# Kernel tuning notes

Hardware: AMD Instinct MI355X
Metric: run time of the kernel (lower is better)

The kernel has to match this reference:

```python
import jax, jax.numpy as jnp
import numpy as np

N, E, F_IN, HID, H, EDIM, G = 50000, 800000, 64, 32, 4, 4, 1024
NEG = 0.2  # LeakyReLU slope (GATv2Conv default)


def _glorot(key, shape):
    s = jnp.sqrt(6.0 / (shape[0] + shape[-1]))
    return jax.random.uniform(key, shape, minval=-s, maxval=s, dtype=jnp.float32)


def setup_inputs() -> dict:
    key = jax.random.key(0)
    ks = jax.random.split(key, 20)
    d = {}
    d["x"] = jax.random.normal(ks[0], (N, F_IN), dtype=jnp.float32)
    d["edge_index"] = jax.random.randint(ks[1], (2, E), 0, N)
    d["edge_attr"] = jax.random.normal(ks[2], (E, EDIM), dtype=jnp.float32)
    d["batch"] = jnp.sort(jax.random.randint(ks[3], (N,), 0, G))
    dims = [F_IN, HID * H, HID * H]
    i = 4
    for l, din in enumerate(dims, 1):
        d[f"Wl{l}"] = _glorot(ks[i], (din, H * HID)); i += 1
        d[f"bl{l}"] = jnp.zeros((H * HID,), jnp.float32)
        d[f"Wr{l}"] = _glorot(ks[i], (din, H * HID)); i += 1
        d[f"br{l}"] = jnp.zeros((H * HID,), jnp.float32)
        d[f"We{l}"] = _glorot(ks[i], (EDIM, H * HID)); i += 1
        d[f"att{l}"] = _glorot(ks[i], (H, HID)); i += 1
        d[f"bias{l}"] = jnp.zeros((H * HID,), jnp.float32)
    d["Wlin"] = _glorot(ks[i], (H * HID, 1)); i += 1
    d["blin"] = jnp.zeros((1,), jnp.float32)
    return d


def _add_self_loops(edge_index, edge_attr):
    # PyG add_self_loops with fill_value='mean': self-loop edge feature is the
    # mean of incoming-edge features (zeros for isolated targets).
    src0, dst0 = edge_index[0], edge_index[1]
    cnt = jax.ops.segment_sum(jnp.ones((src0.shape[0],), jnp.float32), dst0, num_segments=N)
    loop_attr = jax.ops.segment_sum(edge_attr, dst0, num_segments=N) / jnp.maximum(cnt, 1.0)[:, None]
    ar = jnp.arange(N)
    src = jnp.concatenate([src0, ar])
    dst = jnp.concatenate([dst0, ar])
    ea = jnp.concatenate([edge_attr, loop_attr], axis=0)
    return src, dst, ea


def _gatv2_conv(x, src, dst, ea, Wl, bl, Wr, br, We, att, bias):
    n = x.shape[0]
    xl = (x @ Wl + bl).reshape(n, H, HID)   # source transform (message values)
    xr = (x @ Wr + br).reshape(n, H, HID)   # target transform
    e = jax.nn.leaky_relu(xl[src] + xr[dst] + (ea @ We).reshape(-1, H, HID), NEG)  # [Etot,H,C]
    logit = jnp.einsum('ehc,hc->eh', e, att)
    # segment softmax over destination node (every node has a self-loop)
    m = jax.ops.segment_max(logit, dst, num_segments=n)
    p = jnp.exp(logit - m[dst])
    s = jax.ops.segment_sum(p, dst, num_segments=n)
    alpha = p / (s[dst] + 1e-16)
    out = jax.ops.segment_sum(alpha[:, :, None] * xl[src], dst, num_segments=n)
    return out.reshape(n, H * HID) + bias


def reference(x, edge_index, edge_attr, batch,
              Wl1, bl1, Wr1, br1, We1, att1, bias1,
              Wl2, bl2, Wr2, br2, We2, att2, bias2,
              Wl3, bl3, Wr3, br3, We3, att3, bias3,
              Wlin, blin):
    src, dst, ea = _add_self_loops(edge_index, edge_attr)
    h = jax.nn.relu(_gatv2_conv(x, src, dst, ea, Wl1, bl1, Wr1, br1, We1, att1, bias1))
    h = jax.nn.relu(_gatv2_conv(h, src, dst, ea, Wl2, bl2, Wr2, br2, We2, att2, bias2))
    h = _gatv2_conv(h, src, dst, ea, Wl3, bl3, Wr3, br3, We3, att3, bias3)
    # global mean pool over graphs
    cnt = jax.ops.segment_sum(jnp.ones((N,), jnp.float32), batch, num_segments=G)
    pooled = jax.ops.segment_sum(h, batch, num_segments=G) / jnp.maximum(cnt, 1.0)[:, None]
    # dropout p=0.35 is identity in eval mode
    return pooled @ Wlin + blin
```

## Files before the change

### kernel.cpp

```cpp
#include <hip/hip_runtime.h>
#include <math.h>

#define NN 50000
#define EE 800000
#define FIN 64
#define GG 1024
#define ETOT (EE + NN)
#define PSLOT 16

typedef float v2f __attribute__((ext_vector_type(2)));

__global__ __launch_bounds__(256) void k_init(int* __restrict__ deg, int* __restrict__ fillpos,
    float* __restrict__ psum, int* __restrict__ pcnt) {
  int i = blockIdx.x * 256 + threadIdx.x;
  if (i < NN) { deg[i] = 0; fillpos[i] = 0; }
  if (i < GG * PSLOT) { psum[i] = 0.f; pcnt[i] = 0; }
}

__global__ __launch_bounds__(256) void k_deg(const int* __restrict__ dst, int* __restrict__ deg,
    const int* __restrict__ batch, int* __restrict__ pcnt) {
  int e = blockIdx.x * 256 + threadIdx.x;
  if (e < NN) atomicAdd(&pcnt[(batch[e] << 4) | (e & (PSLOT - 1))], 1);
  if (e >= EE) return;
  atomicAdd(&deg[dst[e]], 1);
}

__global__ __launch_bounds__(256) void k_scan1(const int* __restrict__ deg, int* __restrict__ part) {
  __shared__ int s[256];
  int i = blockIdx.x * 256 + threadIdx.x;
  s[threadIdx.x] = (i < NN) ? deg[i] + 1 : 0;
  __syncthreads();
  for (int st = 128; st > 0; st >>= 1) {
    if (threadIdx.x < st) s[threadIdx.x] += s[threadIdx.x + st];
    __syncthreads();
  }
  if (threadIdx.x == 0) part[blockIdx.x] = s[0];
}

__global__ __launch_bounds__(256) void k_scan2(int* __restrict__ part, int nb, int* __restrict__ offsets) {
  __shared__ int s[256];
  int t = threadIdx.x;
  s[t] = (t < nb) ? part[t] : 0;
  __syncthreads();
  for (int st = 1; st < 256; st <<= 1) {
    int a = (t >= st) ? s[t - st] : 0;
    __syncthreads();
    s[t] += a;
    __syncthreads();
  }
  if (t < nb) part[t] = t ? s[t - 1] : 0;
  if (t == 0) offsets[NN] = ETOT;
}

__global__ __launch_bounds__(256) void k_scan3(const int* __restrict__ deg,
    const int* __restrict__ part, int* __restrict__ offsets) {
  __shared__ int s[256];
  int t = threadIdx.x;
  int i = blockIdx.x * 256 + t;
  int v = (i < NN) ? deg[i] + 1 : 0;
  s[t] = v;
  __syncthreads();
  for (int st = 1; st < 256; st <<= 1) {
    int a = (t >= st) ? s[t - st] : 0;
    __syncthreads();
    s[t] += a;
    __syncthreads();
  }
  if (i < NN) offsets[i] = part[blockIdx.x] + s[t] - v;
}

__global__ __launch_bounds__(256) void k_fill(const int* __restrict__ src,
    const int* __restrict__ dst, const int* __restrict__ offsets,
    const int* __restrict__ deg, int* __restrict__ fillpos,
    int2* __restrict__ pr, float4* __restrict__ csr_ea,
    const float* __restrict__ edge_attr) {
  int i = blockIdx.x * 256 + threadIdx.x;
  if (i < EE) {
    int d = dst[i];
    int p = offsets[d] + atomicAdd(&fillpos[d], 1);
    pr[p] = make_int2(i, src[i]);
    csr_ea[p] = *(const float4*)(edge_attr + (size_t)i * 4);
  } else if (i < EE + NN) {
    int n = i - EE;
    int p = offsets[n] + deg[n];
    pr[p] = make_int2(EE + n, n);
  }
}

__global__ __launch_bounds__(256) void k_selfattr(const int* __restrict__ offsets,
    float4* __restrict__ csr_ea) {
  int wave = threadIdx.x >> 6, lane = threadIdx.x & 63;
  int n = blockIdx.x * 4 + wave;
  if (n >= NN) return;
  int lo = offsets[n], d = offsets[n + 1] - lo - 1;
  float4 s = make_float4(0.f, 0.f, 0.f, 0.f);
  for (int i = lane; i < d; i += 64) {
    float4 v = csr_ea[lo + i];
    s.x += v.x; s.y += v.y; s.z += v.z; s.w += v.w;
  }
  #pragma unroll
  for (int off = 1; off < 64; off <<= 1) {
    s.x += __shfl_xor(s.x, off);
    s.y += __shfl_xor(s.y, off);
    s.z += __shfl_xor(s.z, off);
    s.w += __shfl_xor(s.w, off);
  }
  if (lane == 0) {
    float inv = 1.f / fmaxf((float)d, 1.f);
    csr_ea[lo + d] = make_float4(s.x * inv, s.y * inv, s.z * inv, s.w * inv);
  }
}

__global__ __launch_bounds__(256) void k_gemm(const float* __restrict__ X, int K,
    const float* __restrict__ Wl, const float* __restrict__ bl,
    const float* __restrict__ Wr, const float* __restrict__ br,
    float* __restrict__ xl, float* __restrict__ xr) {
  __shared__ float xsT[128][36];
  int row0 = blockIdx.x * 32;
  int nf4 = 32 * K / 4;
  for (int q = threadIdx.x; q < nf4; q += 256) {
    int r = (q * 4) / K, k0 = (q * 4) % K;
    float4 v = make_float4(0.f, 0.f, 0.f, 0.f);
    int gr = row0 + r;
    if (gr < NN) v = *(const float4*)(X + (size_t)gr * K + k0);
    xsT[k0 + 0][r] = v.x;
    xsT[k0 + 1][r] = v.y;
    xsT[k0 + 2][r] = v.z;
    xsT[k0 + 3][r] = v.w;
  }
  __syncthreads();
  int lane = threadIdx.x & 63, wv = threadIdx.x >> 6;
  int c0 = lane * 4, r0 = wv * 8;
  const float* wbase = (c0 < 128) ? (Wl + c0) : (Wr + c0 - 128);
  v2f acc2[4][4];
  #pragma unroll
  for (int rp = 0; rp < 4; rp++) {
    #pragma unroll
    for (int c = 0; c < 4; c++) acc2[rp][c] = (v2f){0.f, 0.f};
  }
  #pragma unroll 4
  for (int k = 0; k < K; k++) {
    float4 w4 = *(const float4*)(wbase + (size_t)k * 128);
    float4 xa = *(const float4*)&xsT[k][r0];
    float4 xb = *(const float4*)&xsT[k][r0 + 4];
    v2f xp[4] = {{xa.x, xa.y}, {xa.z, xa.w}, {xb.x, xb.y}, {xb.z, xb.w}};
    #pragma unroll
    for (int rp = 0; rp < 4; rp++) {
      acc2[rp][0] += xp[rp] * w4.x;
      acc2[rp][1] += xp[rp] * w4.y;
      acc2[rp][2] += xp[rp] * w4.z;
      acc2[rp][3] += xp[rp] * w4.w;
    }
  }
  float4 b4 = (c0 < 128) ? *(const float4*)(bl + c0) : *(const float4*)(br + c0 - 128);
  float* obase = (c0 < 128) ? (xl + c0) : (xr + c0 - 128);
  #pragma unroll
  for (int rp = 0; rp < 4; rp++) {
    #pragma unroll
    for (int h = 0; h < 2; h++) {
      int gr = row0 + r0 + rp * 2 + h;
      if (gr < NN) {
        float4 o;
        o.x = (h ? acc2[rp][0].y : acc2[rp][0].x) + b4.x;
        o.y = (h ? acc2[rp][1].y : acc2[rp][1].x) + b4.y;
        o.z = (h ? acc2[rp][2].y : acc2[rp][2].x) + b4.z;
        o.w = (h ? acc2[rp][3].y : acc2[rp][3].x) + b4.w;
        *(float4*)(obase + (size_t)gr * 128) = o;
      }
    }
  }
}

__global__ __launch_bounds__(64) void k_attn(
    const float* __restrict__ xl, const float* __restrict__ xr,
    const int* __restrict__ offsets, const int2* __restrict__ pr,
    const float4* __restrict__ csr_ea,
    const float* __restrict__ We, const float* __restrict__ att,
    const float* __restrict__ bias, float* __restrict__ hout, int relu_flag,
    const float* __restrict__ Wlin, const int* __restrict__ batch,
    float* __restrict__ psum) {
  int lane = threadIdx.x & 63;
  int t = blockIdx.x;
  if (t >= NN) return;
  int sub = lane >> 4;
  int cl = lane & 15;
  int ch0 = cl * 8;

  v2f xr2[4], we2[4][4], at2[4];
  {
    float4 a = *(const float4*)(xr + (size_t)t * 128 + ch0);
    float4 b = *(const float4*)(xr + (size_t)t * 128 + ch0 + 4);
    xr2[0] = (v2f){a.x, a.y}; xr2[1] = (v2f){a.z, a.w};
    xr2[2] = (v2f){b.x, b.y}; xr2[3] = (v2f){b.z, b.w};
  }
  #pragma unroll
  for (int k = 0; k < 4; k++) {
    float4 a = *(const float4*)(We + k * 128 + ch0);
    float4 b = *(const float4*)(We + k * 128 + ch0 + 4);
    we2[k][0] = (v2f){a.x, a.y}; we2[k][1] = (v2f){a.z, a.w};
    we2[k][2] = (v2f){b.x, b.y}; we2[k][3] = (v2f){b.z, b.w};
  }
  {
    float4 a = *(const float4*)(att + ch0);
    float4 b = *(const float4*)(att + ch0 + 4);
    at2[0] = (v2f){a.x, a.y}; at2[1] = (v2f){a.z, a.w};
    at2[2] = (v2f){b.x, b.y}; at2[3] = (v2f){b.z, b.w};
  }

  float den = 0.f;
  v2f acc2[4];
  #pragma unroll
  for (int j = 0; j < 4; j++) acc2[j] = (v2f){0.f, 0.f};

  int lo = offsets[t], hi = offsets[t + 1];
  int p = lo + sub;
  int s0 = 0;
  float4 ea0 = make_float4(0.f, 0.f, 0.f, 0.f);
  if (p < hi) { int2 q = pr[p]; s0 = q.y; ea0 = csr_ea[p]; }

  #pragma unroll 1
  for (; p < hi; p += 4) {
    const float* xlb = xl + (size_t)s0 * 128 + ch0;
    float4 xa = *(const float4*)(xlb);
    float4 xb = *(const float4*)(xlb + 4);
    int pn = p + 4;
    int s1 = 0;
    float4 ea1 = make_float4(0.f, 0.f, 0.f, 0.f);
    if (pn < hi) { int2 q = pr[pn]; s1 = q.y; ea1 = csr_ea[pn]; }

    v2f xls2[4] = {{xa.x, xa.y}, {xa.z, xa.w}, {xb.x, xb.y}, {xb.z, xb.w}};
    v2f d2 = (v2f){0.f, 0.f};
    #pragma unroll
    for (int j = 0; j < 4; j++) {
      v2f e2 = xls2[j] + xr2[j];
      e2 += we2[0][j] * ea0.x;
      e2 += we2[1][j] * ea0.y;
      e2 += we2[2][j] * ea0.z;
      e2 += we2[3][j] * ea0.w;
      v2f mx = {fmaxf(e2.x, 0.f), fmaxf(e2.y, 0.f)};
      e2 = e2 * 0.2f + mx * 0.8f;
      d2 += e2 * at2[j];
    }
    float part = d2.x + d2.y;
    part += __shfl_xor(part, 1);
    part += __shfl_xor(part, 2);
    float pe = __expf(part);
    den += pe;
    #pragma unroll
    for (int j = 0; j < 4; j++) acc2[j] += xls2[j] * pe;
    s0 = s1; ea0 = ea1;
  }

  #pragma unroll
  for (int off = 16; off <= 32; off <<= 1) {
    den += __shfl_xor(den, off);
    #pragma unroll
    for (int j = 0; j < 4; j++) {
      v2f o;
      o.x = __shfl_xor(acc2[j].x, off);
      o.y = __shfl_xor(acc2[j].y, off);
      acc2[j] += o;
    }
  }

  if (sub == 0) {
    float inv = 1.f / (den + 1e-16f);
    v2f bs2[4];
    {
      float4 c = *(const float4*)(bias + ch0);
      float4 d = *(const float4*)(bias + ch0 + 4);
      bs2[0] = (v2f){c.x, c.y}; bs2[1] = (v2f){c.z, c.w};
      bs2[2] = (v2f){d.x, d.y}; bs2[3] = (v2f){d.z, d.w};
    }
    v2f o2[4];
    #pragma unroll
    for (int j = 0; j < 4; j++) {
      o2[j] = acc2[j] * inv + bs2[j];
      if (relu_flag) {
        o2[j].x = fmaxf(o2[j].x, 0.f);
        o2[j].y = fmaxf(o2[j].y, 0.f);
      }
    }
    if (psum == nullptr) {
      float* ob = hout + (size_t)t * 128 + ch0;
      *(float4*)(ob) = make_float4(o2[0].x, o2[0].y, o2[1].x, o2[1].y);
      *(float4*)(ob + 4) = make_float4(o2[2].x, o2[2].y, o2[3].x, o2[3].y);
    } else {
      float4 wa = *(const float4*)(Wlin + ch0);
      float4 wb = *(const float4*)(Wlin + ch0 + 4);
      v2f wl2[4] = {{wa.x, wa.y}, {wa.z, wa.w}, {wb.x, wb.y}, {wb.z, wb.w}};
      v2f pd = o2[0] * wl2[0];
      pd += o2[1] * wl2[1];
      pd += o2[2] * wl2[2];
      pd += o2[3] * wl2[3];
      float pv = pd.x + pd.y;
      pv += __shfl_xor(pv, 1);
      pv += __shfl_xor(pv, 2);
      pv += __shfl_xor(pv, 4);
      pv += __shfl_xor(pv, 8);
      if (cl == 0) atomicAdd(&psum[(batch[t] << 4) | (t & (PSLOT - 1))], pv);
    }
  }
}

__global__ __launch_bounds__(256) void k_fin(const float* __restrict__ psum,
    const int* __restrict__ pcnt, const float* __restrict__ blin, float* __restrict__ out) {
  int g = blockIdx.x * 256 + threadIdx.x;
  if (g >= GG) return;
  float s = 0.f;
  int c = 0;
  #pragma unroll
  for (int k = 0; k < PSLOT; k++) {
    s += psum[(g << 4) | k];
    c += pcnt[(g << 4) | k];
  }
  out[g] = s / fmaxf((float)c, 1.f) + blin[0];
}

extern "C" void kernel_launch(void* const* d_in, const int* in_sizes, int n_in,
                              void* d_out, int out_size, void* d_ws, size_t ws_size,
                              hipStream_t stream) {
  const float* x = (const float*)d_in[0];
  const int* ei = (const int*)d_in[1];
  const float* edge_attr = (const float*)d_in[2];
  const int* batch = (const int*)d_in[3];
  const float *Wl[3], *bl[3], *Wr[3], *br[3], *We[3], *att[3], *bias[3];
  for (int l = 0; l < 3; l++) {
    int b = 4 + l * 7;
    Wl[l] = (const float*)d_in[b + 0];
    bl[l] = (const float*)d_in[b + 1];
    Wr[l] = (const float*)d_in[b + 2];
    br[l] = (const float*)d_in[b + 3];
    We[l] = (const float*)d_in[b + 4];
    att[l] = (const float*)d_in[b + 5];
    bias[l] = (const float*)d_in[b + 6];
  }
  const float* Wlin = (const float*)d_in[25];
  const float* blin = (const float*)d_in[26];
  float* out = (float*)d_out;

  const int* src = ei;
  const int* dst = ei + EE;

  char* p = (char*)d_ws;
  size_t used = 0;
  auto carve = [&](size_t bytes) -> void* {
    void* r = p + used;
    used += (bytes + 255) & ~(size_t)255;
    return r;
  };
  int* deg = (int*)carve(NN * sizeof(int));
  int* fillpos = (int*)carve(NN * sizeof(int));
  int* offsets = (int*)carve((NN + 1) * sizeof(int));
  int* part = (int*)carve(256 * sizeof(int));
  int2* pr = (int2*)carve((size_t)ETOT * sizeof(int2));
  float4* csr_ea = (float4*)carve((size_t)ETOT * sizeof(float4));
  float* xl = (float*)carve((size_t)NN * 128 * sizeof(float));
  float* xr = (float*)carve((size_t)NN * 128 * sizeof(float));
  float* hbuf = (float*)carve((size_t)NN * 128 * sizeof(float));
  float* psum = (float*)carve(GG * PSLOT * sizeof(float));
  int* pcnt = (int*)carve(GG * PSLOT * sizeof(int));
  if (used > ws_size) return;

  const int NB = (NN + 255) / 256;

  k_init<<<NB, 256, 0, stream>>>(deg, fillpos, psum, pcnt);
  k_deg<<<(EE + 255) / 256, 256, 0, stream>>>(dst, deg, batch, pcnt);
  k_scan1<<<NB, 256, 0, stream>>>(deg, part);
  k_scan2<<<1, 256, 0, stream>>>(part, NB, offsets);
  k_scan3<<<NB, 256, 0, stream>>>(deg, part, offsets);
  k_fill<<<(EE + NN + 255) / 256, 256, 0, stream>>>(src, dst, offsets, deg, fillpos, pr, csr_ea, edge_attr);

  const int GEMM_NB = (NN + 31) / 32;
  const int NODE_NB = (NN + 3) / 4;

  k_selfattr<<<NODE_NB, 256, 0, stream>>>(offsets, csr_ea);

  k_gemm<<<GEMM_NB, 256, 0, stream>>>(x, FIN, Wl[0], bl[0], Wr[0], br[0], xl, xr);
  k_attn<<<NN, 64, 0, stream>>>(xl, xr, offsets, pr, csr_ea, We[0], att[0], bias[0], hbuf, 1,
                                nullptr, nullptr, nullptr);
  k_gemm<<<GEMM_NB, 256, 0, stream>>>(hbuf, 128, Wl[1], bl[1], Wr[1], br[1], xl, xr);
  k_attn<<<NN, 64, 0, stream>>>(xl, xr, offsets, pr, csr_ea, We[1], att[1], bias[1], hbuf, 1,
                                nullptr, nullptr, nullptr);
  k_gemm<<<GEMM_NB, 256, 0, stream>>>(hbuf, 128, Wl[2], bl[2], Wr[2], br[2], xl, xr);
  k_attn<<<NN, 64, 0, stream>>>(xl, xr, offsets, pr, csr_ea, We[2], att[2], bias[2], nullptr, 0,
                                Wlin, batch, psum);

  k_fin<<<(GG + 255) / 256, 256, 0, stream>>>(psum, pcnt, blin, out);
}
```

Baseline: 453.4 us.

## Fuse self-loop mean attributes into attention and drop CSR edge_attr copy

Removes self-loop entries from the CSR and the permuted edge_attr buffer; the attention kernel gathers edge_attr by original edge id, accumulates the mean incoming attribute, and computes the self-loop contribution at the end. This eliminates the k_selfattr pass and the edge_attr scatter in k_fill. Index prefetching is deepened by one iteration to hide the extra indirection. The trade-off is random 16-byte gathers of edge_attr in each of three layers instead of contiguous reads.

```diff
diff --git a/kernel.cpp b/kernel.cpp
--- a/kernel.cpp
+++ b/kernel.cpp
@@ -5,7 +5,6 @@
 #define EE 800000
 #define FIN 64
 #define GG 1024
-#define ETOT (EE + NN)
 #define PSLOT 16
 
 typedef float v2f __attribute__((ext_vector_type(2)));
@@ -28,7 +27,7 @@
 __global__ __launch_bounds__(256) void k_scan1(const int* __restrict__ deg, int* __restrict__ part) {
   __shared__ int s[256];
   int i = blockIdx.x * 256 + threadIdx.x;
-  s[threadIdx.x] = (i < NN) ? deg[i] + 1 : 0;
+  s[threadIdx.x] = (i < NN) ? deg[i] : 0;
   __syncthreads();
   for (int st = 128; st > 0; st >>= 1) {
     if (threadIdx.x < st) s[threadIdx.x] += s[threadIdx.x + st];
@@ -49,7 +48,7 @@
     __syncthreads();
   }
   if (t < nb) part[t] = t ? s[t - 1] : 0;
-  if (t == 0) offsets[NN] = ETOT;
+  if (t == 0) offsets[NN] = EE;
 }
 
 __global__ __launch_bounds__(256) void k_scan3(const int* __restrict__ deg,
@@ -57,7 +56,7 @@
   __shared__ int s[256];
   int t = threadIdx.x;
   int i = blockIdx.x * 256 + t;
-  int v = (i < NN) ? deg[i] + 1 : 0;
+  int v = (i < NN) ? deg[i] : 0;
   s[t] = v;
   __syncthreads();
   for (int st = 1; st < 256; st <<= 1) {
@@ -71,44 +70,12 @@
 
 __global__ __launch_bounds__(256) void k_fill(const int* __restrict__ src,
     const int* __restrict__ dst, const int* __restrict__ offsets,
-    const int* __restrict__ deg, int* __restrict__ fillpos,
-    int2* __restrict__ pr, float4* __restrict__ csr_ea,
-    const float* __restrict__ edge_attr) {
+    int* __restrict__ fillpos, int2* __restrict__ pr) {
   int i = blockIdx.x * 256 + threadIdx.x;
-  if (i < EE) {
-    int d = dst[i];
-    int p = offsets[d] + atomicAdd(&fillpos[d], 1);
-    pr[p] = make_int2(i, src[i]);
-    csr_ea[p] = *(const float4*)(edge_attr + (size_t)i * 4);
-  } else if (i < EE + NN) {
-    int n = i - EE;
-    int p = offsets[n] + deg[n];
-    pr[p] = make_int2(EE + n, n);
-  }
-}
-
-__global__ __launch_bounds__(256) void k_selfattr(const int* __restrict__ offsets,
-    float4* __restrict__ csr_ea) {
-  int wave = threadIdx.x >> 6, lane = threadIdx.x & 63;
-  int n = blockIdx.x * 4 + wave;
-  if (n >= NN) return;
-  int lo = offsets[n], d = offsets[n + 1] - lo - 1;
-  float4 s = make_float4(0.f, 0.f, 0.f, 0.f);
-  for (int i = lane; i < d; i += 64) {
-    float4 v = csr_ea[lo + i];
-    s.x += v.x; s.y += v.y; s.z += v.z; s.w += v.w;
-  }
-  #pragma unroll
-  for (int off = 1; off < 64; off <<= 1) {
-    s.x += __shfl_xor(s.x, off);
-    s.y += __shfl_xor(s.y, off);
-    s.z += __shfl_xor(s.z, off);
-    s.w += __shfl_xor(s.w, off);
-  }
-  if (lane == 0) {
-    float inv = 1.f / fmaxf((float)d, 1.f);
-    csr_ea[lo + d] = make_float4(s.x * inv, s.y * inv, s.z * inv, s.w * inv);
-  }
+  if (i >= EE) return;
+  int d = dst[i];
+  int p = offsets[d] + atomicAdd(&fillpos[d], 1);
+  pr[p] = make_int2(i, src[i]);
 }
 
 __global__ __launch_bounds__(256) void k_gemm(const float* __restrict__ X, int K,
@@ -174,7 +141,7 @@
 __global__ __launch_bounds__(64) void k_attn(
     const float* __restrict__ xl, const float* __restrict__ xr,
     const int* __restrict__ offsets, const int2* __restrict__ pr,
-    const float4* __restrict__ csr_ea,
+    const float* __restrict__ edge_attr,
     const float* __restrict__ We, const float* __restrict__ att,
     const float* __restrict__ bias, float* __restrict__ hout, int relu_flag,
     const float* __restrict__ Wlin, const int* __restrict__ batch,
@@ -211,35 +178,44 @@
   v2f acc2[4];
   #pragma unroll
   for (int j = 0; j < 4; j++) acc2[j] = (v2f){0.f, 0.f};
+  float4 easum = make_float4(0.f, 0.f, 0.f, 0.f);
 
   int lo = offsets[t], hi = offsets[t + 1];
+  int d = hi - lo;
   int p = lo + sub;
-  int s0 = 0;
+
+  int s0 = 0, s1 = 0, e1 = 0;
   float4 ea0 = make_float4(0.f, 0.f, 0.f, 0.f);
-  if (p < hi) { int2 q = pr[p]; s0 = q.y; ea0 = csr_ea[p]; }
+  if (p < hi) {
+    int2 q = pr[p]; s0 = q.y;
+    ea0 = *(const float4*)(edge_attr + (size_t)q.x * 4);
+  }
+  if (p + 4 < hi) { int2 q = pr[p + 4]; s1 = q.y; e1 = q.x; }
 
   #pragma unroll 1
   for (; p < hi; p += 4) {
     const float* xlb = xl + (size_t)s0 * 128 + ch0;
     float4 xa = *(const float4*)(xlb);
     float4 xb = *(const float4*)(xlb + 4);
-    int pn = p + 4;
-    int s1 = 0;
+    int s2 = 0, e2 = 0;
+    if (p + 8 < hi) { int2 q = pr[p + 8]; s2 = q.y; e2 = q.x; }
     float4 ea1 = make_float4(0.f, 0.f, 0.f, 0.f);
-    if (pn < hi) { int2 q = pr[pn]; s1 = q.y; ea1 = csr_ea[pn]; }
+    if (p + 4 < hi) ea1 = *(const float4*)(edge_attr + (size_t)e1 * 4);
+
+    easum.x += ea0.x; easum.y += ea0.y; easum.z += ea0.z; easum.w += ea0.w;
 
     v2f xls2[4] = {{xa.x, xa.y}, {xa.z, xa.w}, {xb.x, xb.y}, {xb.z, xb.w}};
     v2f d2 = (v2f){0.f, 0.f};
     #pragma unroll
     for (int j = 0; j < 4; j++) {
-      v2f e2 = xls2[j] + xr2[j];
-      e2 += we2[0][j] * ea0.x;
-      e2 += we2[1][j] * ea0.y;
-      e2 += we2[2][j] * ea0.z;
-      e2 += we2[3][j] * ea0.w;
-      v2f mx = {fmaxf(e2.x, 0.f), fmaxf(e2.y, 0.f)};
-      e2 = e2 * 0.2f + mx * 0.8f;
-      d2 += e2 * at2[j];
+      v2f e2v = xls2[j] + xr2[j];
+      e2v += we2[0][j] * ea0.x;
+      e2v += we2[1][j] * ea0.y;
+      e2v += we2[2][j] * ea0.z;
+      e2v += we2[3][j] * ea0.w;
+      v2f mx = {fmaxf(e2v.x, 0.f), fmaxf(e2v.y, 0.f)};
+      e2v = e2v * 0.2f + mx * 0.8f;
+      d2 += e2v * at2[j];
     }
     float part = d2.x + d2.y;
     part += __shfl_xor(part, 1);
@@ -248,12 +224,17 @@
     den += pe;
     #pragma unroll
     for (int j = 0; j < 4; j++) acc2[j] += xls2[j] * pe;
-    s0 = s1; ea0 = ea1;
+
+    s0 = s1; ea0 = ea1; s1 = s2; e1 = e2;
   }
 
   #pragma unroll
   for (int off = 16; off <= 32; off <<= 1) {
     den += __shfl_xor(den, off);
+    easum.x += __shfl_xor(easum.x, off);
+    easum.y += __shfl_xor(easum.y, off);
+    easum.z += __shfl_xor(easum.z, off);
+    easum.w += __shfl_xor(easum.w, off);
     #pragma unroll
     for (int j = 0; j < 4; j++) {
       v2f o;
@@ -263,14 +244,43 @@
     }
   }
 
+  {
+    float invd = 1.f / fmaxf((float)d, 1.f);
+    float m0 = easum.x * invd, m1 = easum.y * invd;
+    float m2 = easum.z * invd, m3 = easum.w * invd;
+    const float* xlb = xl + (size_t)t * 128 + ch0;
+    float4 xa = *(const float4*)(xlb);
+    float4 xb = *(const float4*)(xlb + 4);
+    v2f xlt2[4] = {{xa.x, xa.y}, {xa.z, xa.w}, {xb.x, xb.y}, {xb.z, xb.w}};
+    v2f d2 = (v2f){0.f, 0.f};
+    #pragma unroll
+    for (int j = 0; j < 4; j++) {
+      v2f e2v = xlt2[j] + xr2[j];
+      e2v += we2[0][j] * m0;
+      e2v += we2[1][j] * m1;
+      e2v += we2[2][j] * m2;
+      e2v += we2[3][j] * m3;
+      v2f mx = {fmaxf(e2v.x, 0.f), fmaxf(e2v.y, 0.f)};
+      e2v = e2v * 0.2f + mx * 0.8f;
+      d2 += e2v * at2[j];
+    }
+    float part = d2.x + d2.y;
+    part += __shfl_xor(part, 1);
+    part += __shfl_xor(part, 2);
+    float pe = __expf(part);
+    den += pe;
+    #pragma unroll
+    for (int j = 0; j < 4; j++) acc2[j] += xlt2[j] * pe;
+  }
+
   if (sub == 0) {
-    float inv = 1.f / (den + 1e-16f);
+    float inv = 1.f / den;
     v2f bs2[4];
     {
       float4 c = *(const float4*)(bias + ch0);
-      float4 d = *(const float4*)(bias + ch0 + 4);
+      float4 dd = *(const float4*)(bias + ch0 + 4);
       bs2[0] = (v2f){c.x, c.y}; bs2[1] = (v2f){c.z, c.w};
-      bs2[2] = (v2f){d.x, d.y}; bs2[3] = (v2f){d.z, d.w};
+      bs2[2] = (v2f){dd.x, dd.y}; bs2[3] = (v2f){dd.z, dd.w};
     }
     v2f o2[4];
     #pragma unroll
@@ -353,8 +363,7 @@
   int* fillpos = (int*)carve(NN * sizeof(int));
   int* offsets = (int*)carve((NN + 1) * sizeof(int));
   int* part = (int*)carve(256 * sizeof(int));
-  int2* pr = (int2*)carve((size_t)ETOT * sizeof(int2));
-  float4* csr_ea = (float4*)carve((size_t)ETOT * sizeof(float4));
+  int2* pr = (int2*)carve((size_t)EE * sizeof(int2));
   float* xl = (float*)carve((size_t)NN * 128 * sizeof(float));
   float* xr = (float*)carve((size_t)NN * 128 * sizeof(float));
   float* hbuf = (float*)carve((size_t)NN * 128 * sizeof(float));
@@ -369,21 +378,18 @@
   k_scan1<<<NB, 256, 0, stream>>>(deg, part);
   k_scan2<<<1, 256, 0, stream>>>(part, NB, offsets);
   k_scan3<<<NB, 256, 0, stream>>>(deg, part, offsets);
-  k_fill<<<(EE + NN + 255) / 256, 256, 0, stream>>>(src, dst, offsets, deg, fillpos, pr, csr_ea, edge_attr);
+  k_fill<<<(EE + 255) / 256, 256, 0, stream>>>(src, dst, offsets, fillpos, pr);
 
   const int GEMM_NB = (NN + 31) / 32;
-  const int NODE_NB = (NN + 3) / 4;
-
-  k_selfattr<<<NODE_NB, 256, 0, stream>>>(offsets, csr_ea);
 
   k_gemm<<<GEMM_NB, 256, 0, stream>>>(x, FIN, Wl[0], bl[0], Wr[0], br[0], xl, xr);
-  k_attn<<<NN, 64, 0, stream>>>(xl, xr, offsets, pr, csr_ea, We[0], att[0], bias[0], hbuf, 1,
+  k_attn<<<NN, 64, 0, stream>>>(xl, xr, offsets, pr, edge_attr, We[0], att[0], bias[0], hbuf, 1,
                                 nullptr, nullptr, nullptr);
   k_gemm<<<GEMM_NB, 256, 0, stream>>>(hbuf, 128, Wl[1], bl[1], Wr[1], br[1], xl, xr);
-  k_attn<<<NN, 64, 0, stream>>>(xl, xr, offsets, pr, csr_ea, We[1], att[1], bias[1], hbuf, 1,
+  k_attn<<<NN, 64, 0, stream>>>(xl, xr, offsets, pr, edge_attr, We[1], att[1], bias[1], hbuf, 1,
                                 nullptr, nullptr, nullptr);
   k_gemm<<<GEMM_NB, 256, 0, stream>>>(hbuf, 128, Wl[2], bl[2], Wr[2], br[2], xl, xr);
-  k_attn<<<NN, 64, 0, stream>>>(xl, xr, offsets, pr, csr_ea, We[2], att[2], bias[2], nullptr, 0,
+  k_attn<<<NN, 64, 0, stream>>>(xl, xr, offsets, pr, edge_attr, We[2], att[2], bias[2], nullptr, 0,
                                 Wlin, batch, psum);
 
   k_fin<<<(GG + 255) / 256, 256, 0, stream>>>(psum, pcnt, blin, out);
```

New measurement: 487.9 us. +7.6%, slower.
